# Optimization experiments

Hardware: AMD Instinct MI355X
Metric: run time of the kernel (lower is better)

## Reference

```python
import jax, jax.numpy as jnp
import numpy as np

VOCAB, EDIM, ENC, H, OUT = 50000, 128, 128, 100, 104
B, L, NPT = 128, 64, 64          # batch, statements per seq, nodes per statement tree
N = B * L * NPT                  # 524288 total nodes
MAXD = 6                         # max depth of a 64-node complete binary tree


def setup_inputs() -> dict:
    key = jax.random.key(0)
    ks = jax.random.split(key, 14)
    tokens = jax.random.randint(ks[0], (N,), 0, VOCAB)
    # structured tree topology: each statement tree is a 64-node complete binary tree
    local = np.arange(NPT)
    par_local = np.where(local == 0, 0, (local - 1) // 2)
    depth_local = np.floor(np.log2(local + 1)).astype(np.int32)
    base = np.repeat(np.arange(B * L) * NPT, NPT)
    parent = jnp.asarray(base + np.tile(par_local, B * L), dtype=jnp.int32)
    depth = jnp.asarray(np.tile(depth_local, B * L), dtype=jnp.int32)
    tree_id = jnp.asarray(np.repeat(np.arange(B * L), NPT), dtype=jnp.int32)
    nrm = lambda k, s, sc: jax.random.normal(k, s, jnp.float32) * sc
    return {
        "tokens": tokens, "parent": parent, "depth": depth, "tree_id": tree_id,
        "emb": nrm(ks[1], (VOCAB, EDIM), 0.02),
        "W_lin": nrm(ks[2], (ENC, EDIM), 0.05), "b_lin": nrm(ks[3], (ENC,), 0.05),
        "Wi_f": nrm(ks[4], (3 * H, ENC), 0.05), "Wh_f": nrm(ks[5], (3 * H, H), 0.05),
        "bi_f": nrm(ks[6], (3 * H,), 0.05), "bh_f": nrm(ks[7], (3 * H,), 0.05),
        "Wi_b": nrm(ks[8], (3 * H, ENC), 0.05), "Wh_b": nrm(ks[9], (3 * H, H), 0.05),
        "bi_b": nrm(ks[10], (3 * H,), 0.05), "bh_b": nrm(ks[11], (3 * H,), 0.05),
        "W_fc": nrm(ks[12], (OUT, 2 * H), 0.05), "b_fc": nrm(ks[13], (OUT,), 0.05),
    }


def _gru_scan(x_seq, Wi, Wh, bi, bh):
    # x_seq: [L, B, ENC] -> outputs [L, B, H]. Matches torch.nn.GRU cell math.
    def step(hprev, xt):
        gi = xt @ Wi.T + bi              # [B, 3H]
        gh = hprev @ Wh.T + bh
        ir, iz, inn = jnp.split(gi, 3, axis=-1)
        hr, hz, hn = jnp.split(gh, 3, axis=-1)
        r = jax.nn.sigmoid(ir + hr)
        z = jax.nn.sigmoid(iz + hz)
        n = jnp.tanh(inn + r * hn)
        hnew = (1.0 - z) * n + z * hprev
        return hnew, hnew
    h0 = jnp.zeros((x_seq.shape[1], Wh.shape[1]), x_seq.dtype)
    _, ys = jax.lax.scan(step, h0, x_seq)
    return ys


def reference(tokens, parent, depth, tree_id, emb, W_lin, b_lin,
              Wi_f, Wh_f, bi_f, bh_f, Wi_b, Wh_b, bi_b, bh_b, W_fc, b_fc):
    # per-node value: linear(embedding(token))   [N, ENC]
    h = emb[tokens] @ W_lin.T + b_lin
    # bottom-up subtree sum: h(node) = v(node) + sum(h(children)), batched by depth level
    for d in range(MAXD, 0, -1):
        contrib = jnp.where((depth == d)[:, None], h, 0.0)
        h = h.at[parent].add(contrib)
    # TreeEncoder output: max over all node hidden states of each tree
    encodes = jax.ops.segment_max(h, tree_id, num_segments=B * L)  # [B*L, ENC]
    x = encodes.reshape(B, L, ENC).transpose(1, 0, 2)              # [L, B, ENC]
    yf = _gru_scan(x, Wi_f, Wh_f, bi_f, bh_f)                      # [L, B, H]
    yb = _gru_scan(x[::-1], Wi_b, Wh_b, bi_b, bh_b)[::-1]
    gru_out = jnp.concatenate([yf, yb], axis=-1)                   # [L, B, 2H]
    pooled = gru_out.max(axis=0)                                   # [B, 2H]
    return pooled @ W_fc.T + b_fc                                  # [B, OUT]
```

## Files before the change

kernel.cpp:

```cpp
#include <hip/hip_runtime.h>
#include <hip/hip_bf16.h>

typedef __bf16 bf16_t;
typedef __attribute__((ext_vector_type(8))) __bf16 bf16x8;
typedef __attribute__((ext_vector_type(4))) float f32x4;

#define TREES 8192
#define ENC 128
#define HH 100
#define G3 300
#define GSTRIDE 304
#define BB 128
#define LL 64
#define OUTD 104
#define TPB_TREES 8

__device__ __forceinline__ float sigm(float x) { return 1.0f / (1.0f + __expf(-x)); }
__device__ __forceinline__ float tanh_f(float x) { return 2.0f / (1.0f + __expf(-2.0f * x)) - 1.0f; }
__device__ __forceinline__ float bflo(unsigned int u) { return __builtin_bit_cast(float, u << 16); }
__device__ __forceinline__ float bfhi(unsigned int u) { return __builtin_bit_cast(float, u & 0xffff0000u); }

__device__ __forceinline__ void ldsbar() {
  asm volatile("s_waitcnt lgkmcnt(0)\n\ts_barrier" ::: "memory");
}

__device__ __forceinline__ int subtree_size(int n) {
  int np1 = n + 1;
  int d = 31 - __clz(np1);
  return ((64 >> d) - 1) + (((np1 & (np1 - 1)) == 0) ? 1 : 0);
}

__global__ __launch_bounds__(256) void k0_prep(const float* __restrict__ W_lin,
                                               const float* __restrict__ Wi_f,
                                               const float* __restrict__ Wi_b,
                                               const float* __restrict__ emb,
                                               bf16_t* __restrict__ Wbf,
                                               bf16_t* __restrict__ Wibf,
                                               bf16_t* __restrict__ embbf) {
  int i = blockIdx.x * 256 + threadIdx.x;
  if (i < 1600000) {
    float4 v = ((const float4*)emb)[i];
    ushort4 u;
    u.x = __builtin_bit_cast(unsigned short, (bf16_t)v.x);
    u.y = __builtin_bit_cast(unsigned short, (bf16_t)v.y);
    u.z = __builtin_bit_cast(unsigned short, (bf16_t)v.z);
    u.w = __builtin_bit_cast(unsigned short, (bf16_t)v.w);
    ((ushort4*)embbf)[i] = u;
  }
  if (i < 128 * 128) Wbf[i] = (bf16_t)W_lin[i];
  if (i < 608 * 128) {
    int jg = i >> 7, k = i & 127;
    int dir = (jg >= GSTRIDE) ? 1 : 0;
    int j = jg - dir * GSTRIDE;
    float v = 0.0f;
    if (j < G3) v = dir ? Wi_b[j * 128 + k] : Wi_f[j * 128 + k];
    Wibf[i] = (bf16_t)v;
  }
}

__global__ __launch_bounds__(256) void k1_tree(const int* __restrict__ tokens,
                                               const bf16_t* __restrict__ embbf,
                                               const bf16_t* __restrict__ Wbf,
                                               const float* __restrict__ b_lin,
                                               float* __restrict__ encodes) {
  __shared__ float s_[64][129];
  __shared__ float maxbuf[2][128];
  __shared__ float sb[128];
  int tid = threadIdx.x;
  int wave = tid >> 6;
  int lane = tid & 63;
  int ri = lane & 15;
  int kg = lane >> 4;
  int wm = wave >> 1;
  int wn = wave & 1;

  if (tid < 128) sb[tid] = b_lin[tid];

  bf16x8 bfr[4][4];
#pragma unroll
  for (int ks = 0; ks < 4; ++ks)
#pragma unroll
    for (int ni = 0; ni < 4; ++ni)
      bfr[ks][ni] = *(const bf16x8*)(Wbf + (size_t)((wn * 4 + ni) * 16 + ri) * 128 +
                                     ks * 32 + kg * 8);

  float szs[2][4];
#pragma unroll
  for (int mi = 0; mi < 2; ++mi)
#pragma unroll
    for (int rr = 0; rr < 4; ++rr)
      szs[mi][rr] = (float)subtree_size(wm * 32 + mi * 16 + kg * 4 + rr);

  int n = tid >> 2;
  int q = tid & 3;
  int c = tid >> 1;
  int half = tid & 1;
  int pc = (c & ~31) | ((((c >> 3) + (c >> 5)) & 3) << 3) | (c & 7);
  int tree0 = blockIdx.x * TPB_TREES;

  uint4 pre[4];
  {
    int tok = tokens[tree0 * 64 + n];
    const uint4* src = (const uint4*)(embbf + (size_t)tok * ENC) + q * 4;
#pragma unroll
    for (int i = 0; i < 4; ++i) pre[i] = src[i];
  }
  __syncthreads();

  for (int t = 0; t < TPB_TREES; ++t) {
    int tree = tree0 + t;

#pragma unroll
    for (int i = 0; i < 4; ++i) {
      uint4 p = pre[i];
      float4 f0 = {bflo(p.x), bfhi(p.x), bflo(p.y), bfhi(p.y)};
      float4 f1 = {bflo(p.z), bfhi(p.z), bflo(p.w), bfhi(p.w)};
      int col = q * 32 + (((i + q) & 3) << 3);
      *(float4*)&s_[n][col] = f0;
      *(float4*)&s_[n][col + 4] = f1;
    }

    if (t + 1 < TPB_TREES) {
      int tok = tokens[(tree + 1) * 64 + n];
      const uint4* src = (const uint4*)(embbf + (size_t)tok * ENC) + q * 4;
#pragma unroll
      for (int i = 0; i < 4; ++i) pre[i] = src[i];
    }
    ldsbar();

    if (half == 0) s_[31][pc] += s_[63][pc];
    {
      float r[8];
      int pb = 15 + half * 8;
#pragma unroll
      for (int i = 0; i < 8; ++i) {
        int p = pb + i;
        r[i] = s_[p][pc] + s_[2 * p + 1][pc] + s_[2 * p + 2][pc];
        s_[p][pc] = r[i];
      }
      float tt[4];
      int pb2 = 7 + half * 4;
#pragma unroll
      for (int i = 0; i < 4; ++i) {
        int p = pb2 + i;
        tt[i] = s_[p][pc] + r[2 * i] + r[2 * i + 1];
        s_[p][pc] = tt[i];
      }
      float uu[2];
      int pb3 = 3 + half * 2;
#pragma unroll
      for (int i = 0; i < 2; ++i) {
        int p = pb3 + i;
        uu[i] = s_[p][pc] + tt[2 * i] + tt[2 * i + 1];
        s_[p][pc] = uu[i];
      }
      int p1 = 1 + half;
      float w1 = s_[p1][pc] + uu[0] + uu[1];
      s_[p1][pc] = w1;
      float w2 = __shfl_xor(w1, 1);
      if (half == 0) s_[0][pc] = s_[0][pc] + w1 + w2;
    }
    ldsbar();

    f32x4 acc[2][4];
#pragma unroll
    for (int mi = 0; mi < 2; ++mi)
#pragma unroll
      for (int ni = 0; ni < 4; ++ni) {
        f32x4 z = {0.f, 0.f, 0.f, 0.f};
        acc[mi][ni] = z;
      }
#pragma unroll
    for (int ks = 0; ks < 4; ++ks) {
      int k0p = ks * 32 + (((kg + ks) & 3) << 3);
#pragma unroll
      for (int mi = 0; mi < 2; ++mi) {
        int row = wm * 32 + mi * 16 + ri;
        float4 a0 = *(const float4*)&s_[row][k0p];
        float4 a1 = *(const float4*)&s_[row][k0p + 4];
        bf16x8 afr;
        afr[0] = (bf16_t)a0.x; afr[1] = (bf16_t)a0.y; afr[2] = (bf16_t)a0.z; afr[3] = (bf16_t)a0.w;
        afr[4] = (bf16_t)a1.x; afr[5] = (bf16_t)a1.y; afr[6] = (bf16_t)a1.z; afr[7] = (bf16_t)a1.w;
#pragma unroll
        for (int ni = 0; ni < 4; ++ni)
          acc[mi][ni] = __builtin_amdgcn_mfma_f32_16x16x32_bf16(afr, bfr[ks][ni], acc[mi][ni], 0, 0, 0);
      }
    }

    float cmax[4];
#pragma unroll
    for (int ni = 0; ni < 4; ++ni) {
      float bl = sb[(wn * 4 + ni) * 16 + ri];
      float m = -1e30f;
#pragma unroll
      for (int mi = 0; mi < 2; ++mi) {
        f32x4 a = acc[mi][ni];
        m = fmaxf(m, fmaxf(fmaxf(a.x + szs[mi][0] * bl, a.y + szs[mi][1] * bl),
                           fmaxf(a.z + szs[mi][2] * bl, a.w + szs[mi][3] * bl)));
      }
      cmax[ni] = m;
    }
#pragma unroll
    for (int off = 16; off < 64; off <<= 1) {
#pragma unroll
      for (int ni = 0; ni < 4; ++ni)
        cmax[ni] = fmaxf(cmax[ni], __shfl_xor(cmax[ni], off));
    }
    if (lane < 16) {
#pragma unroll
      for (int ni = 0; ni < 4; ++ni) maxbuf[wm][(wn * 4 + ni) * 16 + lane] = cmax[ni];
    }
    ldsbar();
    if (tid < 128) {
      encodes[(size_t)tree * ENC + tid] = fmaxf(maxbuf[0][tid], maxbuf[1][tid]);
    }
  }
}

__global__ __launch_bounds__(256) void k2_gi(const float* __restrict__ encodes,
                                             const bf16_t* __restrict__ Wibf,
                                             const float* __restrict__ bi_f,
                                             const float* __restrict__ bi_b,
                                             float* __restrict__ GI) {
  int tid = threadIdx.x;
  int wave = tid >> 6;
  int lane = tid & 63;
  int ri = lane & 15;
  int kg = lane >> 4;
  int m0 = blockIdx.x * 16;

  f32x4 acc[10];
#pragma unroll
  for (int i = 0; i < 10; ++i) {
    f32x4 z = {0.f, 0.f, 0.f, 0.f};
    acc[i] = z;
  }

  int r = m0 + ri;
  int er = (r & 127) * 64 + (r >> 7);
  const float* arow = encodes + (size_t)er * ENC;
#pragma unroll
  for (int ks = 0; ks < 4; ++ks) {
    int k0 = ks * 32 + kg * 8;
    float4 a0 = *(const float4*)(arow + k0);
    float4 a1 = *(const float4*)(arow + k0 + 4);
    bf16x8 afr;
    afr[0] = (bf16_t)a0.x; afr[1] = (bf16_t)a0.y; afr[2] = (bf16_t)a0.z; afr[3] = (bf16_t)a0.w;
    afr[4] = (bf16_t)a1.x; afr[5] = (bf16_t)a1.y; afr[6] = (bf16_t)a1.z; afr[7] = (bf16_t)a1.w;
#pragma unroll
    for (int i = 0; i < 10; ++i) {
      int nt = wave + i * 4;
      if (nt < 38) {
        bf16x8 bfr = *(const bf16x8*)(Wibf + (nt * 16 + ri) * 128 + k0);
        acc[i] = __builtin_amdgcn_mfma_f32_16x16x32_bf16(afr, bfr, acc[i], 0, 0, 0);
      }
    }
  }
#pragma unroll
  for (int i = 0; i < 10; ++i) {
    int nt = wave + i * 4;
    if (nt >= 38) continue;
    int jg = nt * 16 + ri;
    int dir = (jg >= GSTRIDE) ? 1 : 0;
    int j = jg - dir * GSTRIDE;
    if (j >= G3) continue;
    float bias = dir ? bi_b[j] : bi_f[j];
#pragma unroll
    for (int rr = 0; rr < 4; ++rr) {
      int rowg = m0 + kg * 4 + rr;
      int l = rowg >> 7, b = rowg & 127;
      GI[(((size_t)dir * LL + l) * BB + b) * GSTRIDE + j] = acc[i][rr] + bias;
    }
  }
}

__global__ __launch_bounds__(640) void k3_gru(const float* __restrict__ GI,
                                              const float* __restrict__ Wh_f,
                                              const float* __restrict__ Wh_b,
                                              const float* __restrict__ bh_f,
                                              const float* __restrict__ bh_b,
                                              float* __restrict__ pooled) {
  int blk = blockIdx.x;
  int dir = blk >> 7;
  int b = blk & 127;
  int tid = threadIdx.x;
  __shared__ __align__(16) float h_lds[104];
  __shared__ float gh_lds[304];
  __shared__ float gi_lds[2][304];
  const float* Wh = dir ? Wh_b : Wh_f;
  const float* bh = dir ? bh_b : bh_f;

  int j = tid >> 1;
  int kg = tid & 1;
  int kbase = kg * 52;
  bool isdot = (tid < 600);

  float4 wv[13];
  float bhj = 0.f;
  if (isdot) {
#pragma unroll
    for (int c = 0; c < 13; ++c) {
      int k0 = kbase + c * 4;
      float4 v;
      v.x = (k0 + 0 < HH) ? Wh[j * HH + k0 + 0] : 0.f;
      v.y = (k0 + 1 < HH) ? Wh[j * HH + k0 + 1] : 0.f;
      v.z = (k0 + 2 < HH) ? Wh[j * HH + k0 + 2] : 0.f;
      v.w = (k0 + 3 < HH) ? Wh[j * HH + k0 + 3] : 0.f;
      wv[c] = v;
    }
    if (kg == 0) bhj = bh[j];
  }
  if (tid < 104) h_lds[tid] = 0.f;

  const float* giB = GI + (size_t)dir * LL * BB * GSTRIDE + (size_t)b * GSTRIDE;
  if (tid < G3) {
    int la0 = dir ? 63 : 0;
    gi_lds[0][tid] = giB[(size_t)la0 * BB * GSTRIDE + tid];
  }
  float ymax = -1e30f;
  __syncthreads();

  for (int step = 0; step < 64; ++step) {
    int cur = step & 1;
    int nxt = cur ^ 1;
    float ginext = 0.f;
    if (tid < G3) {
      int ns = (step < 63) ? step + 1 : 63;
      int la = dir ? (63 - ns) : ns;
      ginext = giB[(size_t)la * BB * GSTRIDE + tid];
    }
    if (isdot) {
      float a0 = 0.f, a1 = 0.f, a2 = 0.f, a3 = 0.f;
#pragma unroll
      for (int c = 0; c < 13; ++c) {
        float4 hv = *(const float4*)&h_lds[kbase + c * 4];
        a0 += wv[c].x * hv.x;
        a1 += wv[c].y * hv.y;
        a2 += wv[c].z * hv.z;
        a3 += wv[c].w * hv.w;
      }
      float p = (a0 + a1) + (a2 + a3);
      p += __shfl_xor(p, 1);
      if (kg == 0) gh_lds[j] = p + bhj;
    }
    __syncthreads();
    if (tid < HH) {
      float r = sigm(gi_lds[cur][tid] + gh_lds[tid]);
      float z = sigm(gi_lds[cur][100 + tid] + gh_lds[100 + tid]);
      float n = tanh_f(gi_lds[cur][200 + tid] + r * gh_lds[200 + tid]);
      float hnew = (1.f - z) * n + z * h_lds[tid];
      ymax = fmaxf(ymax, hnew);
      h_lds[tid] = hnew;
    }
    if (tid < G3 && step < 63) gi_lds[nxt][tid] = ginext;
    __syncthreads();
  }
  if (tid < HH) pooled[(size_t)b * 200 + dir * 100 + tid] = ymax;
}

__global__ __launch_bounds__(128) void k4_fc(const float* __restrict__ pooled,
                                             const float* __restrict__ W_fc,
                                             const float* __restrict__ b_fc,
                                             float* __restrict__ out) {
  int b = blockIdx.x;
  int o = threadIdx.x;
  if (o >= OUTD) return;
  const float* p = pooled + (size_t)b * 200;
  const float* w = W_fc + (size_t)o * 200;
  float acc = b_fc[o];
#pragma unroll 8
  for (int j = 0; j < 200; ++j) acc += p[j] * w[j];
  out[(size_t)b * OUTD + o] = acc;
}

extern "C" void kernel_launch(void* const* d_in, const int* in_sizes, int n_in,
                              void* d_out, int out_size, void* d_ws, size_t ws_size,
                              hipStream_t stream) {
  const int* tokens = (const int*)d_in[0];
  const float* emb = (const float*)d_in[4];
  const float* W_lin = (const float*)d_in[5];
  const float* b_lin = (const float*)d_in[6];
  const float* Wi_f = (const float*)d_in[7];
  const float* Wh_f = (const float*)d_in[8];
  const float* bi_f = (const float*)d_in[9];
  const float* bh_f = (const float*)d_in[10];
  const float* Wi_b = (const float*)d_in[11];
  const float* Wh_b = (const float*)d_in[12];
  const float* bi_b = (const float*)d_in[13];
  const float* bh_b = (const float*)d_in[14];
  const float* W_fc = (const float*)d_in[15];
  const float* b_fc = (const float*)d_in[16];

  float* encodes = (float*)d_ws;
  float* GI = encodes + (size_t)TREES * ENC;
  float* pooled = GI + (size_t)2 * LL * BB * GSTRIDE;
  bf16_t* Wbf = (bf16_t*)(pooled + (size_t)BB * 200);
  bf16_t* Wibf = Wbf + 128 * 128;
  bf16_t* embbf = (bf16_t*)GI;

  k0_prep<<<6250, 256, 0, stream>>>(W_lin, Wi_f, Wi_b, emb, Wbf, Wibf, embbf);
  k1_tree<<<TREES / TPB_TREES, 256, 0, stream>>>(tokens, embbf, Wbf, b_lin, encodes);
  k2_gi<<<512, 256, 0, stream>>>(encodes, Wibf, bi_f, bi_b, GI);
  k3_gru<<<256, 640, 0, stream>>>(GI, Wh_f, Wh_b, bh_f, bh_b, pooled);
  k4_fc<<<BB, 128, 0, stream>>>(pooled, W_fc, b_fc, (float*)d_out);
}
```

Baseline: 142.2 us.

## Repartition tree-kernel MFMA tiles by output column and grid-stride embedding conversion

In the tree kernel, each wave now owns 32 output columns across all 64 rows instead of a 2x2 row/column split. The column max therefore finishes inside one wave, and the LDS maxbuf, its extra barrier-guarded pass and the bias LDS staging are removed. Each wave now loads all A fragments from LDS, so LDS reads and bf16 conversions go up, while B fragment registers drop. Separately, the prep kernel uses 2048 blocks with four strided conversion iterations per thread instead of 6250 blocks; the weight-conversion index ranges still fit inside the smaller grid.

```diff
diff --git a/kernel.cpp b/kernel.cpp
--- a/kernel.cpp
+++ b/kernel.cpp
@@ -38,14 +38,18 @@
                                                bf16_t* __restrict__ Wibf,
                                                bf16_t* __restrict__ embbf) {
   int i = blockIdx.x * 256 + threadIdx.x;
-  if (i < 1600000) {
-    float4 v = ((const float4*)emb)[i];
-    ushort4 u;
-    u.x = __builtin_bit_cast(unsigned short, (bf16_t)v.x);
-    u.y = __builtin_bit_cast(unsigned short, (bf16_t)v.y);
-    u.z = __builtin_bit_cast(unsigned short, (bf16_t)v.z);
-    u.w = __builtin_bit_cast(unsigned short, (bf16_t)v.w);
-    ((ushort4*)embbf)[i] = u;
+#pragma unroll
+  for (int r = 0; r < 4; ++r) {
+    int e = i + r * 524288;
+    if (e < 1600000) {
+      float4 v = ((const float4*)emb)[e];
+      ushort4 u;
+      u.x = __builtin_bit_cast(unsigned short, (bf16_t)v.x);
+      u.y = __builtin_bit_cast(unsigned short, (bf16_t)v.y);
+      u.z = __builtin_bit_cast(unsigned short, (bf16_t)v.z);
+      u.w = __builtin_bit_cast(unsigned short, (bf16_t)v.w);
+      ((ushort4*)embbf)[e] = u;
+    }
   }
   if (i < 128 * 128) Wbf[i] = (bf16_t)W_lin[i];
   if (i < 608 * 128) {
@@ -64,32 +68,30 @@
                                                const float* __restrict__ b_lin,
                                                float* __restrict__ encodes) {
   __shared__ float s_[64][129];
-  __shared__ float maxbuf[2][128];
-  __shared__ float sb[128];
   int tid = threadIdx.x;
   int wave = tid >> 6;
   int lane = tid & 63;
   int ri = lane & 15;
   int kg = lane >> 4;
-  int wm = wave >> 1;
-  int wn = wave & 1;
-
-  if (tid < 128) sb[tid] = b_lin[tid];
-
-  bf16x8 bfr[4][4];
+
+  bf16x8 bfr[4][2];
 #pragma unroll
   for (int ks = 0; ks < 4; ++ks)
 #pragma unroll
-    for (int ni = 0; ni < 4; ++ni)
-      bfr[ks][ni] = *(const bf16x8*)(Wbf + (size_t)((wn * 4 + ni) * 16 + ri) * 128 +
+    for (int ni = 0; ni < 2; ++ni)
+      bfr[ks][ni] = *(const bf16x8*)(Wbf + (size_t)((wave * 2 + ni) * 16 + ri) * 128 +
                                      ks * 32 + kg * 8);
 
-  float szs[2][4];
-#pragma unroll
-  for (int mi = 0; mi < 2; ++mi)
+  float bl[2];
+#pragma unroll
+  for (int ni = 0; ni < 2; ++ni) bl[ni] = b_lin[wave * 32 + ni * 16 + ri];
+
+  float szs[4][4];
+#pragma unroll
+  for (int mi = 0; mi < 4; ++mi)
 #pragma unroll
     for (int rr = 0; rr < 4; ++rr)
-      szs[mi][rr] = (float)subtree_size(wm * 32 + mi * 16 + kg * 4 + rr);
+      szs[mi][rr] = (float)subtree_size(mi * 16 + kg * 4 + rr);
 
   int n = tid >> 2;
   int q = tid & 3;
@@ -105,7 +107,6 @@
 #pragma unroll
     for (int i = 0; i < 4; ++i) pre[i] = src[i];
   }
-  __syncthreads();
 
   for (int t = 0; t < TPB_TREES; ++t) {
     int tree = tree0 + t;
@@ -162,11 +163,11 @@
     }
     ldsbar();
 
-    f32x4 acc[2][4];
-#pragma unroll
-    for (int mi = 0; mi < 2; ++mi)
-#pragma unroll
-      for (int ni = 0; ni < 4; ++ni) {
+    f32x4 acc[4][2];
+#pragma unroll
+    for (int mi = 0; mi < 4; ++mi)
+#pragma unroll
+      for (int ni = 0; ni < 2; ++ni) {
         f32x4 z = {0.f, 0.f, 0.f, 0.f};
         acc[mi][ni] = z;
       }
@@ -174,46 +175,43 @@
     for (int ks = 0; ks < 4; ++ks) {
       int k0p = ks * 32 + (((kg + ks) & 3) << 3);
 #pragma unroll
-      for (int mi = 0; mi < 2; ++mi) {
-        int row = wm * 32 + mi * 16 + ri;
+      for (int mi = 0; mi < 4; ++mi) {
+        int row = mi * 16 + ri;
         float4 a0 = *(const float4*)&s_[row][k0p];
         float4 a1 = *(const float4*)&s_[row][k0p + 4];
         bf16x8 afr;
         afr[0] = (bf16_t)a0.x; afr[1] = (bf16_t)a0.y; afr[2] = (bf16_t)a0.z; afr[3] = (bf16_t)a0.w;
         afr[4] = (bf16_t)a1.x; afr[5] = (bf16_t)a1.y; afr[6] = (bf16_t)a1.z; afr[7] = (bf16_t)a1.w;
 #pragma unroll
-        for (int ni = 0; ni < 4; ++ni)
+        for (int ni = 0; ni < 2; ++ni)
           acc[mi][ni] = __builtin_amdgcn_mfma_f32_16x16x32_bf16(afr, bfr[ks][ni], acc[mi][ni], 0, 0, 0);
       }
     }
 
-    float cmax[4];
-#pragma unroll
-    for (int ni = 0; ni < 4; ++ni) {
-      float bl = sb[(wn * 4 + ni) * 16 + ri];
+    float cm[2];
+#pragma unroll
+    for (int ni = 0; ni < 2; ++ni) {
       float m = -1e30f;
 #pragma unroll
-      for (int mi = 0; mi < 2; ++mi) {
+      for (int mi = 0; mi < 4; ++mi) {
         f32x4 a = acc[mi][ni];
-        m = fmaxf(m, fmaxf(fmaxf(a.x + szs[mi][0] * bl, a.y + szs[mi][1] * bl),
-                           fmaxf(a.z + szs[mi][2] * bl, a.w + szs[mi][3] * bl)));
-      }
-      cmax[ni] = m;
+        m = fmaxf(m, fmaxf(fmaxf(a.x + szs[mi][0] * bl[ni], a.y + szs[mi][1] * bl[ni]),
+                           fmaxf(a.z + szs[mi][2] * bl[ni], a.w + szs[mi][3] * bl[ni])));
+      }
+      cm[ni] = m;
     }
 #pragma unroll
     for (int off = 16; off < 64; off <<= 1) {
 #pragma unroll
-      for (int ni = 0; ni < 4; ++ni)
-        cmax[ni] = fmaxf(cmax[ni], __shfl_xor(cmax[ni], off));
+      for (int ni = 0; ni < 2; ++ni)
+        cm[ni] = fmaxf(cm[ni], __shfl_xor(cm[ni], off));
     }
     if (lane < 16) {
 #pragma unroll
-      for (int ni = 0; ni < 4; ++ni) maxbuf[wm][(wn * 4 + ni) * 16 + lane] = cmax[ni];
+      for (int ni = 0; ni < 2; ++ni)
+        encodes[(size_t)tree * ENC + wave * 32 + ni * 16 + lane] = cm[ni];
     }
     ldsbar();
-    if (tid < 128) {
-      encodes[(size_t)tree * ENC + tid] = fmaxf(maxbuf[0][tid], maxbuf[1][tid]);
-    }
   }
 }
 
@@ -398,7 +396,7 @@
   bf16_t* Wibf = Wbf + 128 * 128;
   bf16_t* embbf = (bf16_t*)GI;
 
-  k0_prep<<<6250, 256, 0, stream>>>(W_lin, Wi_f, Wi_b, emb, Wbf, Wibf, embbf);
+  k0_prep<<<2048, 256, 0, stream>>>(W_lin, Wi_f, Wi_b, emb, Wbf, Wibf, embbf);
   k1_tree<<<TREES / TPB_TREES, 256, 0, stream>>>(tokens, embbf, Wbf, b_lin, encodes);
   k2_gi<<<512, 256, 0, stream>>>(encodes, Wibf, bi_f, bi_b, GI);
   k3_gru<<<256, 640, 0, stream>>>(GI, Wh_f, Wh_b, bh_f, bh_b, pooled);
```

New measurement: 149.5 us. 5.1% more time.
